# Performance work log

Hardware: AMD Instinct MI355X
Metric: run time of the kernel (lower is better)

The kernel has to match this reference:

```python
import jax, jax.numpy as jnp
import numpy as np

WALL_COT = 0.5   # init kwarg wall_cot
N_SEG = 64       # number of distinct segment ids (matches fill_max of segs)
MIN_FRAC = 0.01  # thresholds used in the torch loop


def _nearest_ds(x, He, We):
    """F.interpolate(x, size=(He,We), mode='nearest').squeeze(1) for x:[B,1,H,W].
    torch nearest picks src index floor(dst * H/He)."""
    B, _, H, W = x.shape
    iy = (jnp.arange(He) * H) // He
    ix = (jnp.arange(We) * W) // We
    return x[:, 0][:, iy][:, :, ix]  # [B,He,We]


def setup_inputs() -> dict:
    key = jax.random.key(0)
    ks = jax.random.split(key, 6)
    B, C_img, H, W = 8, 3, 512, 512
    C_feat, He, We = 64, 128, 128
    return {
        "outputs": jax.random.normal(ks[0], (B, C_img, H, W), dtype=jnp.float32),
        "inputs": jax.random.normal(ks[1], (B, C_img, H, W), dtype=jnp.float32),
        "enc1": jax.random.normal(ks[2], (B, C_feat, He, We), dtype=jnp.float32),
        "dec1": jax.random.normal(ks[3], (B, C_feat, He, We), dtype=jnp.float32),
        "masks": jax.random.uniform(ks[4], (B, 1, H, W), dtype=jnp.float32),
        "segs": jax.random.randint(ks[5], (B, 1, H, W), 0, N_SEG, dtype=jnp.int32),
        "confidence": jnp.zeros((1,), dtype=jnp.float32),
        "iteration": 1,
        "epoch": 0,
    }


def reference(outputs, inputs, enc1, dec1, masks, segs, confidence, iteration, epoch):
    B, _, He, We = enc1.shape
    npix = He * We

    # nearest-neighbor downsample of segment ids and cost masks to feature res
    seg_i = _nearest_ds(segs, He, We)            # [B,He,We] int
    mask_i = _nearest_ds(masks, He, We)          # [B,He,We]

    # per-pixel reconstruction error, mean over channels
    reco_error = jnp.mean((enc1 - dec1) ** 2, axis=1)  # [B,He,We]

    # segmented reductions: offset segment ids per batch item -> one flat pass
    flat_seg = (jnp.arange(B, dtype=jnp.int32)[:, None] * N_SEG
                + seg_i.reshape(B, -1)).reshape(-1)       # [B*He*We]
    f32 = reco_error.dtype
    counts = jax.ops.segment_sum(jnp.ones_like(flat_seg, dtype=f32), flat_seg,
                                 num_segments=B * N_SEG)  # [B*N_SEG]
    sum_err = jax.ops.segment_sum(reco_error.reshape(-1), flat_seg,
                                  num_segments=B * N_SEG)
    pos_px = ((mask_i > 0) & (mask_i < WALL_COT)).reshape(-1).astype(f32)
    pos_cnt = jax.ops.segment_sum(pos_px, flat_seg, num_segments=B * N_SEG)

    safe_cnt = jnp.maximum(counts, 1.0)
    mean_err = sum_err / safe_cnt                  # mean reco error per segment
    valid = (counts / npix) >= MIN_FRAC            # torch: skip if count frac < 0.01
    pos_flag = (pos_cnt / safe_cnt) > MIN_FRAC     # torch: pos/counts > 0.01
    sel = (valid & pos_flag).astype(f32)
    # flat_reco_error_pos.mean()
    flat_pos_mean = jnp.sum(mean_err * sel) / jnp.maximum(jnp.sum(sel), 1.0)

    # recovery loss: zero-out targets where mask >= wall_cot, masked mean
    targets = jnp.where(masks >= WALL_COT, jnp.zeros_like(inputs), inputs)  # bcast [B,1,H,W]
    mse_recov = jnp.sum((outputs - targets) ** 2, axis=1, keepdims=True)    # [B,1,H,W]
    m = (masks > 0).astype(f32)
    loss_recov = jnp.sum(mse_recov * m) / jnp.maximum(jnp.sum(m), 1.0)

    return loss_recov + flat_pos_mean
```

## Files before the change

kernel.cpp:

```cpp
#include <hip/hip_runtime.h>
#include <stdint.h>

#define BATCH   8
#define CIMG    3
#define HFULL   512
#define WFULL   512
#define HWFULL  (HFULL * WFULL)
#define CFEAT   64
#define HE      128
#define WE      128
#define HWE     (HE * WE)
#define NSEG    64
#define NBSEG   (BATCH * NSEG)
#define WALL_COT 0.5f
#define MIN_FRAC 0.01f

#define NBLK    1024
#define NREP    8

#define WS_BINS_FLOATS (NREP * 3 * NBSEG)
#define WS_BNUM  WS_BINS_FLOATS
#define WS_BDEN  (WS_BNUM + NBLK)
#define WS_ZERO_FLOATS WS_BINS_FLOATS

typedef float vf4 __attribute__((ext_vector_type(4)));

__global__ __launch_bounds__(256) void confloss_main_kernel(
    const float* __restrict__ outputs, const float* __restrict__ inputs,
    const float* __restrict__ enc1,    const float* __restrict__ dec1,
    const float* __restrict__ masks,   const int* __restrict__ segs,
    float* __restrict__ ws)
{
    const int tid = threadIdx.x;
    const int w   = tid >> 6;
    const int l   = tid & 63;
    const int i   = blockIdx.x * 256 + tid;

    __shared__ float s_sumW[4][NSEG];
    __shared__ float s_cnt[NSEG], s_pos[NSEG];
    __shared__ float s_rn[4], s_rd[4];
    s_sumW[w][l] = 0.f;
    if (tid < NSEG) { s_cnt[tid] = 0.f; s_pos[tid] = 0.f; }
    __syncthreads();

    const int g  = i & 32767;
    const int c  = i >> 15;
    const int ba = g >> 12;
    const int ra = (g & 4095) * 4;
    const size_t abase = ((size_t)ba * CFEAT + (size_t)c * 4) * HWE + ra;
    const float* ep0 = enc1 + abase;
    const float* dp0 = dec1 + abase;
    const float* ep1 = ep0 + (size_t)32 * HWE;
    const float* dp1 = dp0 + (size_t)32 * HWE;

    const int bb = i >> 16;
    const int rb = (i & 65535) * 4;
    const float* ob0 = outputs + (size_t)bb * (CIMG * HWFULL) + rb;
    const float* ib0 = inputs  + (size_t)bb * (CIMG * HWFULL) + rb;
    const float* ob1 = ob0 + (size_t)4 * (CIMG * HWFULL);
    const float* ib1 = ib0 + (size_t)4 * (CIMG * HWFULL);
    const float* mp0 = masks + (size_t)bb * HWFULL + rb;
    const float* mp1 = mp0 + (size_t)4 * HWFULL;

    const int ya = ra >> 7, xa = ra & (WE - 1);
    const int fb = ba * HWFULL + (ya * 4) * WFULL + xa * 4;
    const int gl = g & 15;
    const bool duty = (gl == c) || (gl == c + 8);

    const vf4 e00 = *(const vf4*)(ep0);
    const vf4 e01 = *(const vf4*)(ep0 + HWE);
    const vf4 e02 = *(const vf4*)(ep0 + 2 * HWE);
    const vf4 e03 = *(const vf4*)(ep0 + 3 * HWE);
    const vf4 d00 = *(const vf4*)(dp0);
    const vf4 d01 = *(const vf4*)(dp0 + HWE);
    const vf4 d02 = *(const vf4*)(dp0 + 2 * HWE);
    const vf4 d03 = *(const vf4*)(dp0 + 3 * HWE);
    const vf4 mB0 = *(const vf4*)(mp0);
    const vf4 o00 = *(const vf4*)(ob0);
    const vf4 o01 = *(const vf4*)(ob0 + HWFULL);
    const vf4 o02 = *(const vf4*)(ob0 + 2 * HWFULL);
    const vf4 i00 = *(const vf4*)(ib0);
    const vf4 i01 = *(const vf4*)(ib0 + HWFULL);
    const vf4 i02 = *(const vf4*)(ib0 + 2 * HWFULL);
    const int s0 = segs[fb], s1 = segs[fb + 4], s2 = segs[fb + 8], s3 = segs[fb + 12];
    float mk0 = 1.f, mk1 = 1.f, mk2 = 1.f, mk3 = 1.f;
    if (duty) {
        mk0 = masks[fb];     mk1 = masks[fb + 4];
        mk2 = masks[fb + 8]; mk3 = masks[fb + 12];
    }
    asm volatile("" ::
        "v"(e00), "v"(e01), "v"(e02), "v"(e03),
        "v"(d00), "v"(d01), "v"(d02), "v"(d03),
        "v"(mB0), "v"(o00), "v"(o01), "v"(o02),
        "v"(i00), "v"(i01), "v"(i02));
    asm volatile("" :: "v"(s0), "v"(s1), "v"(s2), "v"(s3),
                       "v"(mk0), "v"(mk1), "v"(mk2), "v"(mk3));

    const vf4 e10 = *(const vf4*)(ep1);
    const vf4 e11 = *(const vf4*)(ep1 + HWE);
    const vf4 e12 = *(const vf4*)(ep1 + 2 * HWE);
    const vf4 e13 = *(const vf4*)(ep1 + 3 * HWE);
    const vf4 d10 = *(const vf4*)(dp1);
    const vf4 d11 = *(const vf4*)(dp1 + HWE);
    const vf4 d12 = *(const vf4*)(dp1 + 2 * HWE);
    const vf4 d13 = *(const vf4*)(dp1 + 3 * HWE);
    const vf4 mB1 = *(const vf4*)(mp1);
    const vf4 o10 = *(const vf4*)(ob1);
    const vf4 o11 = *(const vf4*)(ob1 + HWFULL);
    const vf4 o12 = *(const vf4*)(ob1 + 2 * HWFULL);
    const vf4 i10 = *(const vf4*)(ib1);
    const vf4 i11 = *(const vf4*)(ib1 + HWFULL);
    const vf4 i12 = *(const vf4*)(ib1 + 2 * HWFULL);
    asm volatile("" ::
        "v"(e10), "v"(e11), "v"(e12), "v"(e13),
        "v"(d10), "v"(d11), "v"(d12), "v"(d13),
        "v"(mB1), "v"(o10), "v"(o11), "v"(o12),
        "v"(i10), "v"(i11), "v"(i12));

    float num = 0.f, den = 0.f;
#define BPIX(mv, a0, a1, a2, b0, b1, b2)                                   \
    {                                                                       \
        float tgt, dd, mse = 0.f;                                           \
        tgt = ((mv) >= WALL_COT) ? 0.f : (b0); dd = (a0) - tgt; mse += dd*dd; \
        tgt = ((mv) >= WALL_COT) ? 0.f : (b1); dd = (a1) - tgt; mse += dd*dd; \
        tgt = ((mv) >= WALL_COT) ? 0.f : (b2); dd = (a2) - tgt; mse += dd*dd; \
        if ((mv) > 0.f) { num += mse; den += 1.f; }                         \
    }
    BPIX(mB0.x, o00.x, o01.x, o02.x, i00.x, i01.x, i02.x)
    BPIX(mB0.y, o00.y, o01.y, o02.y, i00.y, i01.y, i02.y)
    BPIX(mB0.z, o00.z, o01.z, o02.z, i00.z, i01.z, i02.z)
    BPIX(mB0.w, o00.w, o01.w, o02.w, i00.w, i01.w, i02.w)
    BPIX(mB1.x, o10.x, o11.x, o12.x, i10.x, i11.x, i12.x)
    BPIX(mB1.y, o10.y, o11.y, o12.y, i10.y, i11.y, i12.y)
    BPIX(mB1.z, o10.z, o11.z, o12.z, i10.z, i11.z, i12.z)
    BPIX(mB1.w, o10.w, o11.w, o12.w, i10.w, i11.w, i12.w)
#undef BPIX

    {
        float t0, t1, t2, t3, u0, u1, u2, u3;
#define APIX(f)                                                             \
        t0 = e00.f - d00.f; t1 = e01.f - d01.f;                             \
        t2 = e02.f - d02.f; t3 = e03.f - d03.f;                             \
        u0 = e10.f - d10.f; u1 = e11.f - d11.f;                             \
        u2 = e12.f - d12.f; u3 = e13.f - d13.f;
        APIX(x)
        const float p0 = (t0*t0 + t1*t1 + t2*t2 + t3*t3 +
                          u0*u0 + u1*u1 + u2*u2 + u3*u3) * (1.0f / (float)CFEAT);
        APIX(y)
        const float p1 = (t0*t0 + t1*t1 + t2*t2 + t3*t3 +
                          u0*u0 + u1*u1 + u2*u2 + u3*u3) * (1.0f / (float)CFEAT);
        APIX(z)
        const float p2 = (t0*t0 + t1*t1 + t2*t2 + t3*t3 +
                          u0*u0 + u1*u1 + u2*u2 + u3*u3) * (1.0f / (float)CFEAT);
        APIX(w)
        const float p3 = (t0*t0 + t1*t1 + t2*t2 + t3*t3 +
                          u0*u0 + u1*u1 + u2*u2 + u3*u3) * (1.0f / (float)CFEAT);
#undef APIX
        atomicAdd(&s_sumW[w][s0], p0);
        atomicAdd(&s_sumW[w][s1], p1);
        atomicAdd(&s_sumW[w][s2], p2);
        atomicAdd(&s_sumW[w][s3], p3);
        if (duty) {
            atomicAdd(&s_cnt[s0], 1.f); if (mk0 > 0.f && mk0 < WALL_COT) atomicAdd(&s_pos[s0], 1.f);
            atomicAdd(&s_cnt[s1], 1.f); if (mk1 > 0.f && mk1 < WALL_COT) atomicAdd(&s_pos[s1], 1.f);
            atomicAdd(&s_cnt[s2], 1.f); if (mk2 > 0.f && mk2 < WALL_COT) atomicAdd(&s_pos[s2], 1.f);
            atomicAdd(&s_cnt[s3], 1.f); if (mk3 > 0.f && mk3 < WALL_COT) atomicAdd(&s_pos[s3], 1.f);
        }
    }

#pragma unroll
    for (int off = 32; off >= 1; off >>= 1) {
        num += __shfl_down(num, off);
        den += __shfl_down(den, off);
    }
    if (l == 0) { s_rn[w] = num; s_rd[w] = den; }
    __syncthreads();

    if (tid == 0) {
        ws[WS_BNUM + blockIdx.x] = s_rn[0] + s_rn[1] + s_rn[2] + s_rn[3];
        ws[WS_BDEN + blockIdx.x] = s_rd[0] + s_rd[1] + s_rd[2] + s_rd[3];
    }
    if (tid < NSEG) {
        const int rep = blockIdx.x & (NREP - 1);
        float* bins = ws + rep * (3 * NBSEG);
        const int gb = ba * NSEG + tid;
        const float sv = s_sumW[0][tid] + s_sumW[1][tid] + s_sumW[2][tid] + s_sumW[3][tid];
        if (sv != 0.f) atomicAdd(&bins[NBSEG + gb], sv);
        const float cv = s_cnt[tid];
        if (cv != 0.f) atomicAdd(&bins[gb], cv);
        const float pv = s_pos[tid];
        if (pv != 0.f) atomicAdd(&bins[2 * NBSEG + gb], pv);
    }
}

__global__ __launch_bounds__(512) void confloss_finalize_kernel(
    const float* __restrict__ ws, float* __restrict__ out)
{
    const int t = threadIdx.x;
    float rn = 0.f, rd = 0.f;
#pragma unroll
    for (int k = 0; k < NBLK / 512; ++k) {
        rn += ws[WS_BNUM + t + k * 512];
        rd += ws[WS_BDEN + t + k * 512];
    }
    float cnt = 0.f, sum = 0.f, pos = 0.f;
#pragma unroll
    for (int rep = 0; rep < NREP; ++rep) {
        const float* bins = ws + rep * (3 * NBSEG);
        cnt += bins[t];
        sum += bins[NBSEG + t];
        pos += bins[2 * NBSEG + t];
    }
    const float safe = fmaxf(cnt, 1.0f);
    const float mean = sum / safe;
    const bool valid = (cnt / (float)HWE) >= MIN_FRAC;
    const bool posf  = (pos / safe) > MIN_FRAC;
    float sel = (valid && posf) ? 1.0f : 0.0f;
    float val = mean * sel;

#pragma unroll
    for (int off = 32; off >= 1; off >>= 1) {
        val += __shfl_down(val, off);
        sel += __shfl_down(sel, off);
        rn  += __shfl_down(rn,  off);
        rd  += __shfl_down(rd,  off);
    }
    __shared__ float sv[8], ss[8], sn[8], sd[8];
    const int wid = t >> 6;
    if ((t & 63) == 0) { sv[wid] = val; ss[wid] = sel; sn[wid] = rn; sd[wid] = rd; }
    __syncthreads();
    if (t == 0) {
        float tv = 0.f, ts = 0.f, tn = 0.f, td = 0.f;
#pragma unroll
        for (int k = 0; k < 8; ++k) { tv += sv[k]; ts += ss[k]; tn += sn[k]; td += sd[k]; }
        const float flat_pos_mean = tv / fmaxf(ts, 1.0f);
        const float loss_recov = tn / fmaxf(td, 1.0f);
        out[0] = loss_recov + flat_pos_mean;
    }
}

extern "C" void kernel_launch(void* const* d_in, const int* in_sizes, int n_in,
                              void* d_out, int out_size, void* d_ws, size_t ws_size,
                              hipStream_t stream) {
    const float* outputs = (const float*)d_in[0];
    const float* inputs  = (const float*)d_in[1];
    const float* enc1    = (const float*)d_in[2];
    const float* dec1    = (const float*)d_in[3];
    const float* masks   = (const float*)d_in[4];
    const int*   segs    = (const int*)d_in[5];
    float* ws  = (float*)d_ws;
    float* out = (float*)d_out;

    hipMemsetAsync(ws, 0, WS_ZERO_FLOATS * sizeof(float), stream);

    confloss_main_kernel<<<NBLK, 256, 0, stream>>>(
        outputs, inputs, enc1, dec1, masks, segs, ws);
    confloss_finalize_kernel<<<1, 512, 0, stream>>>(ws, out);
}
```

Measured before the change: 36.99 us.

## Replace global atomic bins with per-block partial records and drop memset

Each block now writes its per-segment counts, error sums and positive counts, plus its recovery partial sums, into its own slot in the workspace. The finalize kernel sums the 128 blocks that belong to each batch item. This removes the workspace memset and the contended global float atomics. Count and positive-pixel histograms in shared memory become per-wave, which also lets the initial block barrier go. In exchange, the single-block finalize does more serial global loads, 128 records per thread.

```diff
diff --git a/kernel.cpp b/kernel.cpp
--- a/kernel.cpp
+++ b/kernel.cpp
@@ -16,12 +16,7 @@
 #define MIN_FRAC 0.01f
 
 #define NBLK    1024
-#define NREP    8
-
-#define WS_BINS_FLOATS (NREP * 3 * NBSEG)
-#define WS_BNUM  WS_BINS_FLOATS
-#define WS_BDEN  (WS_BNUM + NBLK)
-#define WS_ZERO_FLOATS WS_BINS_FLOATS
+#define RECF    208
 
 typedef float vf4 __attribute__((ext_vector_type(4)));
 
@@ -37,11 +32,10 @@
     const int i   = blockIdx.x * 256 + tid;
 
     __shared__ float s_sumW[4][NSEG];
-    __shared__ float s_cnt[NSEG], s_pos[NSEG];
+    __shared__ float s_cntW[4][NSEG];
+    __shared__ float s_posW[4][NSEG];
     __shared__ float s_rn[4], s_rd[4];
-    s_sumW[w][l] = 0.f;
-    if (tid < NSEG) { s_cnt[tid] = 0.f; s_pos[tid] = 0.f; }
-    __syncthreads();
+    s_sumW[w][l] = 0.f; s_cntW[w][l] = 0.f; s_posW[w][l] = 0.f;
 
     const int g  = i & 32767;
     const int c  = i >> 15;
@@ -161,10 +155,10 @@
         atomicAdd(&s_sumW[w][s2], p2);
         atomicAdd(&s_sumW[w][s3], p3);
         if (duty) {
-            atomicAdd(&s_cnt[s0], 1.f); if (mk0 > 0.f && mk0 < WALL_COT) atomicAdd(&s_pos[s0], 1.f);
-            atomicAdd(&s_cnt[s1], 1.f); if (mk1 > 0.f && mk1 < WALL_COT) atomicAdd(&s_pos[s1], 1.f);
-            atomicAdd(&s_cnt[s2], 1.f); if (mk2 > 0.f && mk2 < WALL_COT) atomicAdd(&s_pos[s2], 1.f);
-            atomicAdd(&s_cnt[s3], 1.f); if (mk3 > 0.f && mk3 < WALL_COT) atomicAdd(&s_pos[s3], 1.f);
+            atomicAdd(&s_cntW[w][s0], 1.f); if (mk0 > 0.f && mk0 < WALL_COT) atomicAdd(&s_posW[w][s0], 1.f);
+            atomicAdd(&s_cntW[w][s1], 1.f); if (mk1 > 0.f && mk1 < WALL_COT) atomicAdd(&s_posW[w][s1], 1.f);
+            atomicAdd(&s_cntW[w][s2], 1.f); if (mk2 > 0.f && mk2 < WALL_COT) atomicAdd(&s_posW[w][s2], 1.f);
+            atomicAdd(&s_cntW[w][s3], 1.f); if (mk3 > 0.f && mk3 < WALL_COT) atomicAdd(&s_posW[w][s3], 1.f);
         }
     }
 
@@ -176,41 +170,40 @@
     if (l == 0) { s_rn[w] = num; s_rd[w] = den; }
     __syncthreads();
 
+    float* rec = ws + (size_t)blockIdx.x * RECF;
+    if (tid < NSEG) {
+        const float cv = s_cntW[0][tid] + s_cntW[1][tid] + s_cntW[2][tid] + s_cntW[3][tid];
+        const float sv = s_sumW[0][tid] + s_sumW[1][tid] + s_sumW[2][tid] + s_sumW[3][tid];
+        const float pv = s_posW[0][tid] + s_posW[1][tid] + s_posW[2][tid] + s_posW[3][tid];
+        rec[tid]       = cv;
+        rec[64 + tid]  = sv;
+        rec[128 + tid] = pv;
+    }
     if (tid == 0) {
-        ws[WS_BNUM + blockIdx.x] = s_rn[0] + s_rn[1] + s_rn[2] + s_rn[3];
-        ws[WS_BDEN + blockIdx.x] = s_rd[0] + s_rd[1] + s_rd[2] + s_rd[3];
-    }
-    if (tid < NSEG) {
-        const int rep = blockIdx.x & (NREP - 1);
-        float* bins = ws + rep * (3 * NBSEG);
-        const int gb = ba * NSEG + tid;
-        const float sv = s_sumW[0][tid] + s_sumW[1][tid] + s_sumW[2][tid] + s_sumW[3][tid];
-        if (sv != 0.f) atomicAdd(&bins[NBSEG + gb], sv);
-        const float cv = s_cnt[tid];
-        if (cv != 0.f) atomicAdd(&bins[gb], cv);
-        const float pv = s_pos[tid];
-        if (pv != 0.f) atomicAdd(&bins[2 * NBSEG + gb], pv);
+        rec[192] = s_rn[0] + s_rn[1] + s_rn[2] + s_rn[3];
+        rec[193] = s_rd[0] + s_rd[1] + s_rd[2] + s_rd[3];
     }
 }
 
 __global__ __launch_bounds__(512) void confloss_finalize_kernel(
     const float* __restrict__ ws, float* __restrict__ out)
 {
-    const int t = threadIdx.x;
-    float rn = 0.f, rd = 0.f;
-#pragma unroll
-    for (int k = 0; k < NBLK / 512; ++k) {
-        rn += ws[WS_BNUM + t + k * 512];
-        rd += ws[WS_BDEN + t + k * 512];
-    }
+    const int t  = threadIdx.x;
+    const int b  = t >> 6;
+    const int sg = t & 63;
+
     float cnt = 0.f, sum = 0.f, pos = 0.f;
-#pragma unroll
-    for (int rep = 0; rep < NREP; ++rep) {
-        const float* bins = ws + rep * (3 * NBSEG);
-        cnt += bins[t];
-        sum += bins[NBSEG + t];
-        pos += bins[2 * NBSEG + t];
-    }
+#pragma unroll 8
+    for (int k = 0; k < 128; ++k) {
+        const int blk = (k & 15) | (b << 4) | ((k >> 4) << 7);
+        const float* rec = ws + (size_t)blk * RECF;
+        cnt += rec[sg];
+        sum += rec[64 + sg];
+        pos += rec[128 + sg];
+    }
+    float rn = ws[(size_t)(2 * t) * RECF + 192] + ws[(size_t)(2 * t + 1) * RECF + 192];
+    float rd = ws[(size_t)(2 * t) * RECF + 193] + ws[(size_t)(2 * t + 1) * RECF + 193];
+
     const float safe = fmaxf(cnt, 1.0f);
     const float mean = sum / safe;
     const bool valid = (cnt / (float)HWE) >= MIN_FRAC;
@@ -251,8 +244,6 @@
     float* ws  = (float*)d_ws;
     float* out = (float*)d_out;
 
-    hipMemsetAsync(ws, 0, WS_ZERO_FLOATS * sizeof(float), stream);
-
     confloss_main_kernel<<<NBLK, 256, 0, stream>>>(
         outputs, inputs, enc1, dec1, masks, segs, ws);
     confloss_finalize_kernel<<<1, 512, 0, stream>>>(ws, out);
```

After: 37.84 us. +2.3%, slower.
